# Optimization experiments

Measured on AMD Instinct MI355X. Metric: run time of the kernel, lower is better.

Reference implementation:

```python
import jax, jax.numpy as jnp
import numpy as np

B, T, C, H = 4, 2048, 1024, 16
HD = C // H  # head_dim = 64

def setup_inputs() -> dict:
    key = jax.random.key(0)
    k1, k2, k3 = jax.random.split(key, 3)
    x = jax.random.normal(k1, (B, T, C), dtype=jnp.float32)
    w_qkv = jax.random.normal(k2, (C, 3 * C), dtype=jnp.float32) * (C ** -0.5)
    b_qkv = jnp.zeros((3 * C,), dtype=jnp.float32)
    w_proj = jax.random.normal(k3, (C, C), dtype=jnp.float32) * (C ** -0.5)
    b_proj = jnp.zeros((C,), dtype=jnp.float32)
    return {"x": x, "w_qkv": w_qkv, "b_qkv": b_qkv, "w_proj": w_proj, "b_proj": b_proj}

def reference(x, w_qkv, b_qkv, w_proj, b_proj):
    # QKV projection
    qkv = x @ w_qkv + b_qkv                      # [B,T,3C]
    q, k, v = jnp.split(qkv, 3, axis=-1)         # each [B,T,C]
    # split heads -> [B,H,T,HD]
    q = q.reshape(B, T, H, HD).transpose(0, 2, 1, 3)
    k = k.reshape(B, T, H, HD).transpose(0, 2, 1, 3)
    v = v.reshape(B, T, H, HD).transpose(0, 2, 1, 3)
    # muP attention: scale by 1/head_dim (not 1/sqrt)
    att = jnp.einsum('bhqd,bhkd->bhqk', q, k) * (1.0 / HD)  # [B,H,T,T]
    causal = jnp.tril(jnp.ones((T, T), dtype=bool))
    att = jnp.where(causal[None, None], att, -jnp.inf)
    att = jax.nn.softmax(att, axis=-1)
    # dropout = 0.0 (identity)
    y = jnp.einsum('bhqk,bhkd->bhqd', att, v)    # [B,H,T,HD]
    y = y.transpose(0, 2, 1, 3).reshape(B, T, C)
    y = y @ w_proj + b_proj
    return y
```

## Files before the change

### kernel.cpp

```cpp
#include <hip/hip_runtime.h>
#include <hip/hip_bf16.h>
#include <math.h>

typedef unsigned short ushort_t;
typedef unsigned int uint_t;
typedef __attribute__((ext_vector_type(8))) short short8;
typedef __attribute__((ext_vector_type(4))) float floatx4;
typedef __attribute__((ext_vector_type(2))) uint_t uint2v;

#define BB 4
#define TT 2048
#define CCH 1024
#define HH 16
#define HDIM 64
#define MROWS (BB * TT)

#define GLDS(g, l)                                                        \
  __builtin_amdgcn_global_load_lds(                                       \
      (const __attribute__((address_space(1))) void*)(g),                 \
      (__attribute__((address_space(3))) void*)(l), 16, 0, 0)

#if __has_builtin(__builtin_amdgcn_exp2f)
#define EXP2(x) __builtin_amdgcn_exp2f(x)
#else
#define EXP2(x) exp2f(x)
#endif

__device__ __forceinline__ ushort_t f2bf(float f) {
  union { float f; uint_t u; } x;
  x.f = f;
  uint_t u = x.u;
  u += 0x7FFFu + ((u >> 16) & 1u);
  return (ushort_t)(u >> 16);
}

__device__ __forceinline__ float bf2f(ushort_t v) {
  union { uint_t u; float f; } x;
  x.u = ((uint_t)v) << 16;
  return x.f;
}

__device__ __forceinline__ uint_t pk_trunc(float a, float b) {
  union { float f; uint_t u; } xa, xb;
  xa.f = a; xb.f = b;
  return (xa.u >> 16) | (xb.u & 0xFFFF0000u);
}

__device__ __forceinline__ uint_t pk_rne(float a, float b) {
  return (uint_t)f2bf(a) | ((uint_t)f2bf(b) << 16);
}

__global__ void detect_dtype(const uint_t* __restrict__ x, uint_t* __restrict__ flag) {
  __shared__ int cnt;
  if (threadIdx.x == 0) cnt = 0;
  __syncthreads();
  int c = 0;
  for (int i = threadIdx.x; i < 1024; i += 256) {
    uint_t w = x[i];
    uint_t e = (w >> 7) & 0xFFu;
    if (e >= 100u && e <= 150u) c++;
  }
  atomicAdd(&cnt, c);
  __syncthreads();
  if (threadIdx.x == 0) *flag = (cnt > 512) ? 1u : 0u;
}

__global__ void prep_x(const void* __restrict__ x, ushort_t* __restrict__ xb,
                       const uint_t* __restrict__ flag, int n) {
  int i = blockIdx.x * 256 + threadIdx.x;
  if (i >= n) return;
  if (*flag)
    xb[i] = ((const ushort_t*)x)[i];
  else
    xb[i] = f2bf(((const float*)x)[i]);
}

__global__ __launch_bounds__(256) void prep_wT(const void* __restrict__ w,
                                               ushort_t* __restrict__ wT,
                                               const uint_t* __restrict__ flag,
                                               int N) {
  __shared__ float tile[64][65];
  const int tid = threadIdx.x;
  const int bn = blockIdx.x * 64;
  const int bk = blockIdx.y * 64;
  if (*flag == 0) {
    const float* src = (const float*)w;
#pragma unroll
    for (int p = 0; p < 4; p++) {
      int r = p * 16 + (tid >> 4);
      int c = (tid & 15) * 4;
      float4 v = *(const float4*)&src[(size_t)(bk + r) * N + bn + c];
      tile[r][c] = v.x; tile[r][c + 1] = v.y;
      tile[r][c + 2] = v.z; tile[r][c + 3] = v.w;
    }
  } else {
    const ushort_t* src = (const ushort_t*)w;
#pragma unroll
    for (int p = 0; p < 4; p++) {
      int r = p * 16 + (tid >> 4);
      int c = (tid & 15) * 4;
      const ushort_t* s = &src[(size_t)(bk + r) * N + bn + c];
      tile[r][c] = bf2f(s[0]); tile[r][c + 1] = bf2f(s[1]);
      tile[r][c + 2] = bf2f(s[2]); tile[r][c + 3] = bf2f(s[3]);
    }
  }
  __syncthreads();
#pragma unroll
  for (int p = 0; p < 8; p++) {
    int nn = p * 8 + (tid >> 5);
    int kk = (tid & 31) * 2;
    uint_t u = pk_rne(tile[kk][nn], tile[kk + 1][nn]);
    *(uint_t*)&wT[(size_t)(bn + nn) * 1024 + bk + kk] = u;
  }
}

template <int MODE>
__global__ __launch_bounds__(256) void gemm_bt(
    const ushort_t* __restrict__ A, const ushort_t* __restrict__ Bt,
    const void* __restrict__ bias,
    ushort_t* __restrict__ q_out, ushort_t* __restrict__ k_out,
    ushort_t* __restrict__ v_out, void* __restrict__ outp,
    const uint_t* __restrict__ flag) {
  alignas(16) __shared__ ushort_t As[128 * 32];
  alignas(16) __shared__ ushort_t Bs[128 * 32];

  const int tid = threadIdx.x;
  const int wave = tid >> 6, lane = tid & 63;
  const int quad = lane >> 4, l16 = lane & 15;
  const int wm = (wave & 1) * 64, wn = (wave >> 1) * 64;
  const int bm = blockIdx.x * 128, bn = blockIdx.y * 128;

  floatx4 acc[4][4] = {};

  for (int k0 = 0; k0 < 1024; k0 += 32) {
#pragma unroll
    for (int s = 0; s < 2; s++) {
      int c = tid + s * 256;
      int row = c >> 2, cc = (c & 3) * 8;
      GLDS(&A[(size_t)(bm + row) * 1024 + k0 + cc], &As[c * 8]);
      GLDS(&Bt[(size_t)(bn + row) * 1024 + k0 + cc], &Bs[c * 8]);
    }
    __syncthreads();

    short8 af[4], bf[4];
#pragma unroll
    for (int i = 0; i < 4; i++)
      af[i] = *(const short8*)&As[(wm + i * 16 + l16) * 32 + quad * 8];
#pragma unroll
    for (int i = 0; i < 4; i++)
      bf[i] = *(const short8*)&Bs[(wn + i * 16 + l16) * 32 + quad * 8];

#pragma unroll
    for (int mi = 0; mi < 4; mi++)
#pragma unroll
      for (int ni = 0; ni < 4; ni++)
        acc[mi][ni] = __builtin_amdgcn_mfma_f32_16x16x32_bf16(
            af[mi], bf[ni], acc[mi][ni], 0, 0, 0);
    __syncthreads();
  }

  const bool inbf = (*flag != 0);

#pragma unroll
  for (int mi = 0; mi < 4; mi++) {
#pragma unroll
    for (int ni = 0; ni < 4; ni++) {
#pragma unroll
      for (int r = 0; r < 4; r++) {
        int row = bm + wm + mi * 16 + quad * 4 + r;
        int col = bn + wn + ni * 16 + l16;
        float bsv = inbf ? bf2f(((const ushort_t*)bias)[col])
                         : ((const float*)bias)[col];
        float v = acc[mi][ni][r] + bsv;
        if (MODE == 0) {
          ushort_t bv = f2bf(v);
          int b = row >> 11, t = row & 2047;
          int which = col >> 10, rem = col & 1023;
          int h = rem >> 6, d = rem & 63;
          size_t bh = (size_t)(b * HH + h);
          if (which == 0)
            q_out[(bh * TT + t) * HDIM + d] = bv;
          else if (which == 1)
            k_out[(bh * TT + t) * HDIM + d] = bv;
          else
            v_out[(bh * HDIM + d) * TT + t] = bv;
        } else {
          size_t idx = (size_t)row * CCH + col;
          if (inbf)
            ((ushort_t*)outp)[idx] = f2bf(v);
          else
            ((float*)outp)[idx] = v;
        }
      }
    }
  }
}

__global__ __launch_bounds__(256, 3) void flash_attn(
    const ushort_t* __restrict__ qb, const ushort_t* __restrict__ kb,
    const ushort_t* __restrict__ vtb, ushort_t* __restrict__ attb) {
  alignas(16) __shared__ ushort_t Ks[2][64 * 64];
  alignas(16) __shared__ ushort_t Vs[2][64 * 64];
  alignas(16) __shared__ ushort_t Ps[4][32 * 72];

  const int tid = threadIdx.x;
  const int wave = tid >> 6, lane = tid & 63;
  const int quad = lane >> 4, l16 = lane & 15;
  const int bh = blockIdx.x;
  const int b = bh >> 4, h = bh & 15;
  const int qt = 15 - blockIdx.y;
  const int qbs = qt * 128 + wave * 32;

  const ushort_t* Q = qb + (size_t)bh * TT * HDIM;
  const ushort_t* K = kb + (size_t)bh * TT * HDIM;
  const ushort_t* Vt = vtb + (size_t)bh * HDIM * TT;
  ushort_t* Pw = Ps[wave];

  const float SC = 0.015625f * 1.44269504089f;

  short8 qf[2][2];
#pragma unroll
  for (int m = 0; m < 2; m++)
#pragma unroll
    for (int ks = 0; ks < 2; ks++) {
      short8 a = *(const short8*)&Q[(size_t)(qbs + m * 16 + l16) * HDIM +
                                    ks * 32 + quad * 8];
#pragma unroll
      for (int j = 0; j < 8; j++)
        a[j] = (short)f2bf(bf2f((ushort_t)a[j]) * SC);
      qf[m][ks] = a;
    }

  short8 ones;
#pragma unroll
  for (int j = 0; j < 8; j++) ones[j] = (short)0x3F80;

  floatx4 o[2][4] = {};
  floatx4 osum[2] = {};

  const int lt = (qbs + 31) >> 6;
  const int ntiles = 2 * qt + 2;
  int cur = 0;

#pragma unroll
  for (int s2 = 0; s2 < 2; s2++) {
    int c = tid + s2 * 256;
    int row = c >> 3, gc = ((c & 7) ^ (row & 7)) * 8;
    GLDS(&K[(size_t)row * HDIM + gc], &Ks[0][c * 8]);
    GLDS(&Vt[(size_t)row * TT + gc], &Vs[0][c * 8]);
  }

  for (int kt = 0; kt < ntiles; kt++) {
    const int kt0 = kt * 64;
    cur = kt & 1;
    __syncthreads();

    if (kt + 1 < ntiles) {
      const int n0 = kt0 + 64;
#pragma unroll
      for (int s2 = 0; s2 < 2; s2++) {
        int c = tid + s2 * 256;
        int row = c >> 3, gc = ((c & 7) ^ (row & 7)) * 8;
        GLDS(&K[(size_t)(n0 + row) * HDIM + gc], &Ks[cur ^ 1][c * 8]);
        GLDS(&Vt[(size_t)row * TT + n0 + gc], &Vs[cur ^ 1][c * 8]);
      }
    }

    if (kt > lt) continue;

    short8 kf[4][2];
#pragma unroll
    for (int sub = 0; sub < 4; sub++)
#pragma unroll
      for (int ks = 0; ks < 2; ks++) {
        int col = (ks * 32 + quad * 8) ^ ((l16 & 7) * 8);
        kf[sub][ks] = *(const short8*)&Ks[cur][(sub * 16 + l16) * 64 + col];
      }

#pragma unroll
    for (int m = 0; m < 2; m++) {
      floatx4 s[4] = {};
      __builtin_amdgcn_s_setprio(1);
#pragma unroll
      for (int sub = 0; sub < 4; sub++)
#pragma unroll
        for (int ks = 0; ks < 2; ks++)
          s[sub] = __builtin_amdgcn_mfma_f32_16x16x32_bf16(
              kf[sub][ks], qf[m][ks], s[sub], 0, 0, 0);
      __builtin_amdgcn_s_setprio(0);

      const bool full = (kt0 + 63 <= qbs + m * 16);
      const int qrow = qbs + m * 16 + l16;
#pragma unroll
      for (int sub = 0; sub < 4; sub++) {
#pragma unroll
        for (int r = 0; r < 4; r++) {
          float p = EXP2(s[sub][r]);
          if (!full) {
            int key = kt0 + sub * 16 + quad * 4 + r;
            p = (key <= qrow) ? p : 0.0f;
          }
          s[sub][r] = p;
        }
        uint2v u;
        u[0] = pk_trunc(s[sub][0], s[sub][1]);
        u[1] = pk_trunc(s[sub][2], s[sub][3]);
        *(uint2v*)&Pw[(m * 16 + l16) * 72 + sub * 16 + quad * 4] = u;
      }
    }

    short8 pf[2][2];
#pragma unroll
    for (int m = 0; m < 2; m++)
#pragma unroll
      for (int ks = 0; ks < 2; ks++)
        pf[m][ks] =
            *(const short8*)&Pw[(m * 16 + l16) * 72 + ks * 32 + quad * 8];

    __builtin_amdgcn_s_setprio(1);
#pragma unroll
    for (int m = 0; m < 2; m++)
#pragma unroll
      for (int ks = 0; ks < 2; ks++)
        osum[m] = __builtin_amdgcn_mfma_f32_16x16x32_bf16(
            ones, pf[m][ks], osum[m], 0, 0, 0);

#pragma unroll
    for (int n = 0; n < 4; n++) {
#pragma unroll
      for (int ks = 0; ks < 2; ks++) {
        int col = (ks * 32 + quad * 8) ^ ((l16 & 7) * 8);
        short8 vf = *(const short8*)&Vs[cur][(n * 16 + l16) * 64 + col];
#pragma unroll
        for (int m = 0; m < 2; m++)
          o[m][n] = __builtin_amdgcn_mfma_f32_16x16x32_bf16(
              vf, pf[m][ks], o[m][n], 0, 0, 0);
      }
    }
    __builtin_amdgcn_s_setprio(0);
  }

#pragma unroll
  for (int m = 0; m < 2; m++) {
    float inv = 1.0f / osum[m][0];
    ushort_t* base =
        &attb[((size_t)(b * TT + qbs + m * 16 + l16)) * CCH + h * HDIM];
#pragma unroll
    for (int n = 0; n < 4; n++) {
      uint2v u;
      u[0] = pk_rne(o[m][n][0] * inv, o[m][n][1] * inv);
      u[1] = pk_rne(o[m][n][2] * inv, o[m][n][3] * inv);
      *(uint2v*)&base[n * 16 + quad * 4] = u;
    }
  }
}

extern "C" void kernel_launch(void* const* d_in, const int* in_sizes, int n_in,
                              void* d_out, int out_size, void* d_ws, size_t ws_size,
                              hipStream_t stream) {
  const void* x      = d_in[0];
  const void* w_qkv  = d_in[1];
  const void* b_qkv  = d_in[2];
  const void* w_proj = d_in[3];
  const void* b_proj = d_in[4];

  ushort_t* ws = (ushort_t*)d_ws;
  ushort_t* xb     = ws;
  ushort_t* wqkvT  = ws + 8388608;
  ushort_t* wprojT = ws + 11534336;
  ushort_t* qb     = ws + 12582912;
  ushort_t* kb     = ws + 20971520;
  ushort_t* attb   = xb;
  uint_t*   flag   = (uint_t*)(ws + 29360128);
  ushort_t* vtb    = (ushort_t*)d_out;

  detect_dtype<<<dim3(1), dim3(256), 0, stream>>>((const uint_t*)x, flag);

  prep_x<<<dim3((MROWS * CCH) / 256), dim3(256), 0, stream>>>(
      x, xb, flag, MROWS * CCH);
  prep_wT<<<dim3(48, 16), dim3(256), 0, stream>>>(w_qkv, wqkvT, flag, 3 * CCH);
  prep_wT<<<dim3(16, 16), dim3(256), 0, stream>>>(w_proj, wprojT, flag, CCH);

  gemm_bt<0><<<dim3(MROWS / 128, (3 * CCH) / 128), dim3(256), 0, stream>>>(
      xb, wqkvT, b_qkv, qb, kb, vtb, nullptr, flag);

  flash_attn<<<dim3(BB * HH, 16), dim3(256), 0, stream>>>(qb, kb, vtb, attb);

  gemm_bt<1><<<dim3(MROWS / 128, CCH / 128), dim3(256), 0, stream>>>(
      attb, wprojT, b_proj, nullptr, nullptr, nullptr, d_out, flag);
}
```

Before: 284.6 us.

## Triple-buffer GEMM LDS tiles with async prefetch, XOR swizzle, and MFMA priority

New measurement: 278.6 us. 2.1% less time.

```diff
diff --git a/kernel.cpp b/kernel.cpp
--- a/kernel.cpp
+++ b/kernel.cpp
@@ -115,14 +115,14 @@
 }
 
 template <int MODE>
-__global__ __launch_bounds__(256) void gemm_bt(
+__global__ __launch_bounds__(256, 3) void gemm_bt(
     const ushort_t* __restrict__ A, const ushort_t* __restrict__ Bt,
     const void* __restrict__ bias,
     ushort_t* __restrict__ q_out, ushort_t* __restrict__ k_out,
     ushort_t* __restrict__ v_out, void* __restrict__ outp,
     const uint_t* __restrict__ flag) {
-  alignas(16) __shared__ ushort_t As[128 * 32];
-  alignas(16) __shared__ ushort_t Bs[128 * 32];
+  alignas(16) __shared__ ushort_t As[3][128 * 32];
+  alignas(16) __shared__ ushort_t Bs[3][128 * 32];
 
   const int tid = threadIdx.x;
   const int wave = tid >> 6, lane = tid & 63;
@@ -130,34 +130,63 @@
   const int wm = (wave & 1) * 64, wn = (wave >> 1) * 64;
   const int bm = blockIdx.x * 128, bn = blockIdx.y * 128;
 
+  const int r0 = tid >> 2;
+  const int co = ((tid & 3) ^ ((tid >> 3) & 3)) * 8;
+  const int xs = (quad ^ ((l16 >> 1) & 3)) * 8;
+
   floatx4 acc[4][4] = {};
 
-  for (int k0 = 0; k0 < 1024; k0 += 32) {
-#pragma unroll
-    for (int s = 0; s < 2; s++) {
-      int c = tid + s * 256;
-      int row = c >> 2, cc = (c & 3) * 8;
-      GLDS(&A[(size_t)(bm + row) * 1024 + k0 + cc], &As[c * 8]);
-      GLDS(&Bt[(size_t)(bn + row) * 1024 + k0 + cc], &Bs[c * 8]);
-    }
-    __syncthreads();
+#define STAGE_G(kt, bf_)                                                     \
+  do {                                                                       \
+    const int k0_ = (kt) * 32;                                               \
+    GLDS(&A[(size_t)(bm + r0) * 1024 + k0_ + co], &As[bf_][tid * 8]);        \
+    GLDS(&A[(size_t)(bm + r0 + 64) * 1024 + k0_ + co],                       \
+         &As[bf_][(tid + 256) * 8]);                                         \
+    GLDS(&Bt[(size_t)(bn + r0) * 1024 + k0_ + co], &Bs[bf_][tid * 8]);       \
+    GLDS(&Bt[(size_t)(bn + r0 + 64) * 1024 + k0_ + co],                      \
+         &Bs[bf_][(tid + 256) * 8]);                                         \
+  } while (0)
+
+  STAGE_G(0, 0);
+  STAGE_G(1, 1);
+  STAGE_G(2, 2);
+
+  int buf = 0;
+  for (int kt = 0; kt < 32; kt++) {
+    if (kt <= 29)
+      asm volatile("s_waitcnt vmcnt(8)" ::: "memory");
+    else if (kt == 30)
+      asm volatile("s_waitcnt vmcnt(4)" ::: "memory");
+    else
+      asm volatile("s_waitcnt vmcnt(0)" ::: "memory");
+    __builtin_amdgcn_s_barrier();
+    __builtin_amdgcn_sched_barrier(0);
 
     short8 af[4], bf[4];
 #pragma unroll
     for (int i = 0; i < 4; i++)
-      af[i] = *(const short8*)&As[(wm + i * 16 + l16) * 32 + quad * 8];
+      af[i] = *(const short8*)&As[buf][(wm + i * 16 + l16) * 32 + xs];
 #pragma unroll
     for (int i = 0; i < 4; i++)
-      bf[i] = *(const short8*)&Bs[(wn + i * 16 + l16) * 32 + quad * 8];
-
+      bf[i] = *(const short8*)&Bs[buf][(wn + i * 16 + l16) * 32 + xs];
+    asm volatile("s_waitcnt lgkmcnt(0)" ::: "memory");
+    __builtin_amdgcn_sched_barrier(0);
+    __builtin_amdgcn_s_barrier();
+
+    if (kt + 3 < 32) STAGE_G(kt + 3, buf);
+
+    __builtin_amdgcn_s_setprio(1);
 #pragma unroll
     for (int mi = 0; mi < 4; mi++)
 #pragma unroll
       for (int ni = 0; ni < 4; ni++)
         acc[mi][ni] = __builtin_amdgcn_mfma_f32_16x16x32_bf16(
             af[mi], bf[ni], acc[mi][ni], 0, 0, 0);
-    __syncthreads();
-  }
+    __builtin_amdgcn_s_setprio(0);
+
+    buf = (buf == 2) ? 0 : buf + 1;
+  }
+#undef STAGE_G
 
   const bool inbf = (*flag != 0);
 
```
